# Kernel tuning notes

Measured on AMD Instinct MI355X. Metric: run time of the kernel, lower is better.

Reference implementation:

```python
import jax, jax.numpy as jnp
import numpy as np

EPS = 1e-6
TOP_K = 2


def setup_inputs() -> dict:
    key = jax.random.key(0)
    k0, k1, k2, k3, k4 = jax.random.split(key, 5)
    B, S, H, I, E = 1, 2048, 1024, 3584, 8
    return {
        "hidden_states": jax.random.normal(k0, (B, S, H), jnp.float32),
        "rms_weight": jnp.ones((H,), jnp.float32),
        "gate_w": jax.random.normal(k1, (E, H), jnp.float32) * (H ** -0.5),
        "w1": jax.random.normal(k2, (E, I, H), jnp.float32) * (H ** -0.5),
        "w2": jax.random.normal(k3, (E, H, I), jnp.float32) * (I ** -0.5),
        "w3": jax.random.normal(k4, (E, I, H), jnp.float32) * (H ** -0.5),
    }


def reference(hidden_states, rms_weight, gate_w, w1, w2, w3):
    B, S, H = hidden_states.shape
    E = gate_w.shape[0]
    # RMSNorm (fp32 internally, matches _RMSNorm)
    x = hidden_states.astype(jnp.float32)
    var = jnp.mean(x * x, axis=-1, keepdims=True)
    h = rms_weight * (x * jax.lax.rsqrt(var + EPS))  # [B,S,H]
    # Router: softmax over experts, top-k, renormalize
    logits = jnp.einsum('bsh,eh->bse', h, gate_w)
    scores = jax.nn.softmax(logits.astype(jnp.float32), axis=-1)
    top_w, top_i = jax.lax.top_k(scores, TOP_K)        # [B,S,K]
    top_w = top_w / jnp.sum(top_w, axis=-1, keepdims=True)
    top_w = top_w.astype(h.dtype)
    # Per-token combine weight for every expert: cw[t,e]
    hf = h.reshape(-1, H)                               # [T,H]
    oh = jax.nn.one_hot(top_i.reshape(-1, TOP_K), E, dtype=h.dtype)  # [T,K,E]
    cw = jnp.einsum('tke,tk->te', oh, top_w.reshape(-1, TOP_K))       # [T,E]
    # SwiGLU expert MLPs, batched over experts (dense dispatch; weights zero out unrouted tokens)
    a = jnp.einsum('th,eih->eti', hf, w1)               # [E,T,I]
    g = jnp.einsum('th,eih->eti', hf, w3)               # [E,T,I]
    eo = jnp.einsum('eti,ehi->eth', jax.nn.silu(a) * g, w2)  # [E,T,H]
    out = jnp.einsum('eth,te->th', eo, cw)              # [T,H]
    return hidden_states + out.reshape(B, S, H)
```

## Files before the change

kernel.cpp:

```cpp
#include <hip/hip_runtime.h>
#include <hip/hip_bf16.h>
#include <stdint.h>

#define T_TOK 2048
#define HDIM  1024
#define IDIM  3584
#define NEXP  8
#define NROWS 4096
#define WELEM 29360128
#define NJOBS 40
#define CVTB  512

typedef __attribute__((ext_vector_type(8))) short bf16x8;
typedef __attribute__((ext_vector_type(4))) float f32x4;

typedef __attribute__((address_space(3))) unsigned lds_u32;
typedef const __attribute__((address_space(1))) unsigned glb_u32;

#define MFMA16 __builtin_amdgcn_mfma_f32_16x16x32_bf16

__device__ __forceinline__ unsigned short f2bf(float f){
  union { float f; unsigned u; } v; v.f = f;
  unsigned r = v.u + 0x7FFFu + ((v.u >> 16) & 1u);
  return (unsigned short)(r >> 16);
}
__device__ __forceinline__ unsigned cvt2(float a, float b){
  __hip_bfloat162 h = __float22bfloat162_rn(float2{a, b});
  return *reinterpret_cast<unsigned*>(&h);
}
__device__ __forceinline__ bf16x8 pack8(float4 lo, float4 hi){
  union { __hip_bfloat162 b2[4]; bf16x8 v; } u;
  u.b2[0] = __float22bfloat162_rn(float2{lo.x, lo.y});
  u.b2[1] = __float22bfloat162_rn(float2{lo.z, lo.w});
  u.b2[2] = __float22bfloat162_rn(float2{hi.x, hi.y});
  u.b2[3] = __float22bfloat162_rn(float2{hi.z, hi.w});
  return u.v;
}

__global__ __launch_bounds__(256) void k_rms_router(
    const float* __restrict__ x, const float* __restrict__ rmsw,
    const float* __restrict__ gw, unsigned short* __restrict__ h_bf,
    int* __restrict__ topk_i, float* __restrict__ topk_w, int* __restrict__ count)
{
  const int t = blockIdx.x, tid = threadIdx.x;
  const int lane = tid & 63, wid = tid >> 6;
  float4 x4 = reinterpret_cast<const float4*>(x)[t*256 + tid];
  float ss = x4.x*x4.x + x4.y*x4.y + x4.z*x4.z + x4.w*x4.w;
  #pragma unroll
  for (int o = 32; o >= 1; o >>= 1) ss += __shfl_xor(ss, o);
  __shared__ float sred[4];
  __shared__ float slog[32];
  if (lane == 0) sred[wid] = ss;
  __syncthreads();
  float inv = rsqrtf((sred[0]+sred[1]+sred[2]+sred[3]) * (1.0f/HDIM) + 1e-6f);
  float4 w4 = reinterpret_cast<const float4*>(rmsw)[tid];
  float h0 = x4.x*inv*w4.x, h1 = x4.y*inv*w4.y, h2 = x4.z*inv*w4.z, h3 = x4.w*inv*w4.w;
  ushort4 hb; hb.x = f2bf(h0); hb.y = f2bf(h1); hb.z = f2bf(h2); hb.w = f2bf(h3);
  reinterpret_cast<ushort4*>(h_bf)[t*256 + tid] = hb;
  #pragma unroll
  for (int e = 0; e < NEXP; e++){
    float4 g4 = reinterpret_cast<const float4*>(gw)[e*256 + tid];
    float v = h0*g4.x + h1*g4.y + h2*g4.z + h3*g4.w;
    #pragma unroll
    for (int o = 32; o >= 1; o >>= 1) v += __shfl_xor(v, o);
    if (lane == 0) slog[e*4 + wid] = v;
  }
  __syncthreads();
  if (tid == 0){
    float lg[NEXP];
    #pragma unroll
    for (int e = 0; e < NEXP; e++) lg[e] = slog[e*4]+slog[e*4+1]+slog[e*4+2]+slog[e*4+3];
    int i0 = 0;
    for (int e = 1; e < NEXP; e++) if (lg[e] > lg[i0]) i0 = e;
    int i1 = -1;
    for (int e = 0; e < NEXP; e++){ if (e == i0) continue; if (i1 < 0 || lg[e] > lg[i1]) i1 = e; }
    float m  = fmaxf(lg[i0], lg[i1]);
    float e0 = expf(lg[i0]-m), e1 = expf(lg[i1]-m);
    float s  = e0 + e1;
    topk_i[t*2] = i0; topk_i[t*2+1] = i1;
    topk_w[t*2] = e0/s; topk_w[t*2+1] = e1/s;
    atomicAdd(&count[i0], 1); atomicAdd(&count[i1], 1);
  }
}

__global__ void k_scan(const int* __restrict__ count, int* __restrict__ offset,
                       int* __restrict__ jobs){
  if (threadIdx.x == 0){
    int o = 0, L = 0;
    for (int e = 0; e < NEXP; e++){
      offset[e] = o;
      int nrt = (count[e] + 127) >> 7;
      for (int r = 0; r < nrt && L < NJOBS; r++) jobs[L++] = (e << 8) | r;
      o += count[e];
    }
    for (; L < NJOBS; L++) jobs[L] = -1;
  }
}

__global__ __launch_bounds__(256) void k_scatter(
    const int* __restrict__ topk_i, const float* __restrict__ topk_w,
    const int* __restrict__ offset, int* __restrict__ cursor,
    int* __restrict__ token_of_row, float* __restrict__ wrow, int* __restrict__ slot_of)
{
  int t = blockIdx.x*256 + threadIdx.x;
  if (t >= T_TOK) return;
  #pragma unroll
  for (int k = 0; k < 2; k++){
    int e = topk_i[t*2+k];
    int pos = atomicAdd(&cursor[e], 1);
    int row = offset[e] + pos;
    token_of_row[row] = t;
    wrow[row] = topk_w[t*2+k];
    slot_of[t*2+k] = row;
  }
}

__global__ __launch_bounds__(256) void k_cvt(
    const float4* __restrict__ src, uint2* __restrict__ dst, int n4)
{
  int stride = gridDim.x * blockDim.x;
  for (int i = blockIdx.x*blockDim.x + threadIdx.x; i < n4; i += stride){
    float4 v = src[i];
    dst[i] = make_uint2(cvt2(v.x, v.y), cvt2(v.z, v.w));
  }
}

__global__ __launch_bounds__(256, 3) void k_mlp_in(
    const unsigned short* __restrict__ h_bf, const float* __restrict__ w1,
    const float* __restrict__ w3, const int* __restrict__ token_of_row,
    const int* __restrict__ count, const int* __restrict__ offset,
    const int* __restrict__ jobs, unsigned short* __restrict__ act,
    const float4* __restrict__ w2s, uint2* __restrict__ w2d)
{
  const int d = blockIdx.x;
  const int tid = threadIdx.x;
  if (d >= NJOBS*56){
    if (w2d){
      int i0 = (d - NJOBS*56)*256 + tid;
      for (int i = i0; i < WELEM/4; i += CVTB*256){
        float4 v = w2s[i];
        w2d[i] = make_uint2(cvt2(v.x, v.y), cvt2(v.z, v.w));
      }
    }
    return;
  }
  const int p = d % 56;
  const int t = d / 56;
  const int job = jobs[t];
  if (job < 0) return;
  const int e = job >> 8, rt = job & 255;
  const int cnt = count[e];
  const int off = offset[e], row0 = off + rt*128, rend = off + cnt;
  const int col0 = p * 64;
  const int lane = tid & 63, wid = tid >> 6;
  const int wave_r = wid >> 1, wave_c = wid & 1;

  __shared__ __align__(16) char sA [16384];
  __shared__ __align__(16) char sB1[16384];
  __shared__ __align__(16) char sB3[16384];

  const int srow = tid >> 3;
  const int sg   = (tid & 7) ^ (srow & 7);
  const unsigned short* aptr[4];
  #pragma unroll
  for (int j = 0; j < 4; j++){
    int tok = token_of_row[min(row0 + srow + 32*j, NROWS-1)];
    aptr[j] = h_bf + (size_t)tok*HDIM + sg*8;
  }
  const int bl = (tid & 15) ^ ((tid >> 4) & 15);
  const float* b1base = w1 + ((size_t)e*IDIM + col0 + (tid >> 4))*HDIM + bl*4;
  const float* b3base = w3 + ((size_t)e*IDIM + col0 + (tid >> 4))*HDIM + bl*4;

  #define ISSUE(kk) {                                                                \
    _Pragma("unroll")                                                                \
    for (int j = 0; j < 4; j++)                                                      \
      __builtin_amdgcn_global_load_lds((glb_u32*)(const void*)(aptr[j] + (kk)*64),   \
          (lds_u32*)(void*)(sA + j*4096 + tid*16), 16, 0, 0);                        \
    _Pragma("unroll")                                                                \
    for (int j = 0; j < 4; j++){                                                     \
      __builtin_amdgcn_global_load_lds(                                              \
          (glb_u32*)(const void*)(b1base + (size_t)j*16*HDIM + (kk)*64),             \
          (lds_u32*)(void*)(sB1 + j*4096 + tid*16), 16, 0, 0);                       \
      __builtin_amdgcn_global_load_lds(                                              \
          (glb_u32*)(const void*)(b3base + (size_t)j*16*HDIM + (kk)*64),             \
          (lds_u32*)(void*)(sB3 + j*4096 + tid*16), 16, 0, 0);                       \
    } }

  f32x4 acc1[4][2], acc3[4][2];
  #pragma unroll
  for (int m = 0; m < 4; m++)
    #pragma unroll
    for (int n = 0; n < 2; n++){
      acc1[m][n] = (f32x4){0.f,0.f,0.f,0.f};
      acc3[m][n] = (f32x4){0.f,0.f,0.f,0.f};
    }

  for (int kk = 0; kk < HDIM/64; kk++){
    ISSUE(kk);
    __syncthreads();
    #pragma unroll
    for (int ki = 0; ki < 2; ki++){
      bf16x8 af[4];
      #pragma unroll
      for (int m = 0; m < 4; m++){
        int row = wave_r*64 + m*16 + (lane & 15);
        int slot = ki*4 + (lane >> 4);
        af[m] = *reinterpret_cast<const bf16x8*>(sA + row*128 + ((slot ^ (row&7))<<4));
      }
      #pragma unroll
      for (int n = 0; n < 2; n++){
        int c  = wave_c*32 + n*16 + (lane & 15);
        int l0 = ki*8 + (lane >> 4)*2;
        int p0 = (l0     ^ (c & 15)) << 4;
        int p1 = ((l0+1) ^ (c & 15)) << 4;
        float4 lo1 = *reinterpret_cast<const float4*>(sB1 + c*256 + p0);
        float4 hi1 = *reinterpret_cast<const float4*>(sB1 + c*256 + p1);
        float4 lo3 = *reinterpret_cast<const float4*>(sB3 + c*256 + p0);
        float4 hi3 = *reinterpret_cast<const float4*>(sB3 + c*256 + p1);
        bf16x8 b1 = pack8(lo1, hi1);
        bf16x8 b3 = pack8(lo3, hi3);
        #pragma unroll
        for (int m = 0; m < 4; m++){
          acc1[m][n] = MFMA16(af[m], b1, acc1[m][n], 0,0,0);
          acc3[m][n] = MFMA16(af[m], b3, acc3[m][n], 0,0,0);
        }
      }
    }
    __syncthreads();
  }

  const int lcol = lane & 15, lrow4 = (lane >> 4) * 4;
  #pragma unroll
  for (int m = 0; m < 4; m++){
    #pragma unroll
    for (int n = 0; n < 2; n++){
      int gcol = col0 + wave_c*32 + n*16 + lcol;
      #pragma unroll
      for (int r = 0; r < 4; r++){
        int grow = row0 + wave_r*64 + m*16 + lrow4 + r;
        if (grow < rend){
          float a = acc1[m][n][r], g = acc3[m][n][r];
          float sig = 1.0f / (1.0f + __expf(-a));
          act[(size_t)grow*IDIM + gcol] = f2bf(a * sig * g);
        }
      }
    }
  }
  #undef ISSUE
}

__global__ __launch_bounds__(256, 3) void k_mlp_out(
    const unsigned short* __restrict__ act, const unsigned short* __restrict__ w2bf,
    const float* __restrict__ wrow, const int* __restrict__ count,
    const int* __restrict__ offset, const int* __restrict__ jobs,
    float* __restrict__ eo)
{
  const int d = blockIdx.x;
  const int p = d & 15;
  const int t = d >> 4;
  const int job = jobs[t];
  if (job < 0) return;
  const int e = job >> 8, rt = job & 255;
  const int cnt = count[e];
  const int off = offset[e], row0 = off + rt*128, rend = off + cnt;
  const int col0 = p * 64;
  const int tid = threadIdx.x, lane = tid & 63, wid = tid >> 6;
  const int wave_r = wid >> 1, wave_c = wid & 1;

  __shared__ __align__(16) char sA[32768];
  __shared__ __align__(16) char sB[16384];

  const int sr16 = tid >> 4;
  const int sg   = (tid & 15) ^ sr16;

  const unsigned short* aptr[8];
  #pragma unroll
  for (int j = 0; j < 8; j++){
    int r = min(row0 + j*16 + sr16, NROWS-1);
    aptr[j] = act + (size_t)r*IDIM + sg*8;
  }
  const unsigned short* bptr[4];
  #pragma unroll
  for (int j = 0; j < 4; j++){
    int col = col0 + j*16 + sr16;
    bptr[j] = w2bf + (size_t)(e*HDIM + col)*IDIM + sg*8;
  }

  #define ISSUE(kk) {                                                                \
    _Pragma("unroll")                                                                \
    for (int j = 0; j < 8; j++)                                                      \
      __builtin_amdgcn_global_load_lds((glb_u32*)(const void*)(aptr[j] + (kk)*128),  \
          (lds_u32*)(void*)(sA + j*4096 + tid*16), 16, 0, 0);                        \
    _Pragma("unroll")                                                                \
    for (int j = 0; j < 4; j++)                                                      \
      __builtin_amdgcn_global_load_lds((glb_u32*)(const void*)(bptr[j] + (kk)*128),  \
          (lds_u32*)(void*)(sB + j*4096 + tid*16), 16, 0, 0); }

  f32x4 acc[4][2];
  #pragma unroll
  for (int m = 0; m < 4; m++)
    #pragma unroll
    for (int n = 0; n < 2; n++) acc[m][n] = (f32x4){0.f,0.f,0.f,0.f};

  for (int kk = 0; kk < IDIM/128; kk++){
    ISSUE(kk);
    __syncthreads();
    #pragma unroll
    for (int ki = 0; ki < 4; ki++){
      bf16x8 af[4];
      #pragma unroll
      for (int m = 0; m < 4; m++){
        int row = wave_r*64 + m*16 + (lane & 15);
        int slot = ki*4 + (lane >> 4);
        af[m] = *reinterpret_cast<const bf16x8*>(sA + row*256 + ((slot ^ (row&15))<<4));
      }
      #pragma unroll
      for (int n = 0; n < 2; n++){
        int col = wave_c*32 + n*16 + (lane & 15);
        int slot = ki*4 + (lane >> 4);
        bf16x8 fb = *reinterpret_cast<const bf16x8*>(sB + col*256 + ((slot ^ (col&15))<<4));
        #pragma unroll
        for (int m = 0; m < 4; m++)
          acc[m][n] = MFMA16(af[m], fb, acc[m][n], 0,0,0);
      }
    }
    __syncthreads();
  }

  const int lcol = lane & 15, lrow4 = (lane >> 4) * 4;
  #pragma unroll
  for (int m = 0; m < 4; m++){
    #pragma unroll
    for (int n = 0; n < 2; n++){
      int gcol = col0 + wave_c*32 + n*16 + lcol;
      #pragma unroll
      for (int r = 0; r < 4; r++){
        int grow = row0 + wave_r*64 + m*16 + lrow4 + r;
        if (grow < rend){
          eo[(size_t)grow*HDIM + gcol] = acc[m][n][r] * wrow[grow];
        }
      }
    }
  }
  #undef ISSUE
}

__global__ __launch_bounds__(256) void k_combine(
    const float* __restrict__ x, const float* __restrict__ eo,
    const int* __restrict__ slot_of, float* __restrict__ out)
{
  const int t = blockIdx.x, tid = threadIdx.x;
  const int s0 = slot_of[t*2], s1 = slot_of[t*2+1];
  float4 xv = reinterpret_cast<const float4*>(x)[t*256 + tid];
  float4 a  = reinterpret_cast<const float4*>(eo)[s0*256 + tid];
  float4 b  = reinterpret_cast<const float4*>(eo)[s1*256 + tid];
  float4 ov;
  ov.x = xv.x + a.x + b.x;
  ov.y = xv.y + a.y + b.y;
  ov.z = xv.z + a.z + b.z;
  ov.w = xv.w + a.w + b.w;
  reinterpret_cast<float4*>(out)[t*256 + tid] = ov;
}

extern "C" void kernel_launch(void* const* d_in, const int* in_sizes, int n_in,
                              void* d_out, int out_size, void* d_ws, size_t ws_size,
                              hipStream_t stream)
{
  const float* x    = (const float*)d_in[0];
  const float* rmsw = (const float*)d_in[1];
  const float* gw   = (const float*)d_in[2];
  const float* w1   = (const float*)d_in[3];
  const float* w2   = (const float*)d_in[4];
  const float* w3   = (const float*)d_in[5];
  float* out = (float*)d_out;

  char* ws = (char*)d_ws;
  size_t o = 0;
  auto alloc = [&](size_t bytes) -> void* {
    void* p = ws + o;
    o += (bytes + 255) & ~(size_t)255;
    return p;
  };
  unsigned short* h_bf   = (unsigned short*)alloc((size_t)T_TOK*HDIM*2);
  int*   topk_i          = (int*)  alloc(T_TOK*2*4);
  float* topk_w          = (float*)alloc(T_TOK*2*4);
  int*   counters        = (int*)  alloc(64*4);
  int*   jobs            = (int*)  alloc(NJOBS*4);
  int*   token_of_row    = (int*)  alloc(NROWS*4);
  float* wrow            = (float*)alloc(NROWS*4);
  int*   slot_of         = (int*)  alloc(T_TOK*2*4);
  unsigned short* act    = (unsigned short*)alloc((size_t)NROWS*IDIM*2);
  float* eo              = (float*)alloc((size_t)NROWS*HDIM*4);
  int* count  = counters;
  int* cursor = counters + 8;
  int* offset = counters + 16;

  bool havew2 = (ws_size >= o + (size_t)WELEM*2);
  unsigned short* w2bf = (unsigned short*)(ws + o);

  hipMemsetAsync(counters, 0, 64*4, stream);
  k_rms_router<<<T_TOK, 256, 0, stream>>>(x, rmsw, gw, h_bf, topk_i, topk_w, count);
  k_scan<<<1, 64, 0, stream>>>(count, offset, jobs);
  k_scatter<<<(T_TOK+255)/256, 256, 0, stream>>>(topk_i, topk_w, offset, cursor,
                                                 token_of_row, wrow, slot_of);
  k_mlp_in<<<NJOBS*56 + (havew2 ? CVTB : 0), 256, 0, stream>>>(
      h_bf, w1, w3, token_of_row, count, offset, jobs, act,
      (const float4*)w2, havew2 ? (uint2*)w2bf : (uint2*)nullptr);
  if (!havew2)
    k_cvt<<<2048, 256, 0, stream>>>((const float4*)w2, (uint2*)w2bf, WELEM/4);
  k_mlp_out<<<NJOBS*16, 256, 0, stream>>>(act, w2bf, wrow, count, offset, jobs, eo);
  k_combine<<<T_TOK, 256, 0, stream>>>(x, eo, slot_of, out);
}
```

Before: 297.7 us.

## Double-buffer A tiles and prefetch fp32 weights through registers into bf16 LDS

The gate/up expert GEMM kernel now double-buffers the activation tile in LDS using asynchronous global-to-LDS loads. The fp32 w1/w3 tiles are prefetched into registers one K-step ahead and converted to bf16 once when written to LDS. Before, each wave re-read fp32 from LDS and converted it in the inner loop. This halves LDS footprint and traffic for B and overlaps global loads with MFMA work. The custom barrier only waits on lgkmcnt, so it relies on the compiler's vmcnt handling to make sure the async A loads are complete before they are read, which is a correctness risk.

```diff
diff --git a/kernel.cpp b/kernel.cpp
--- a/kernel.cpp
+++ b/kernel.cpp
@@ -35,6 +35,13 @@
   u.b2[2] = __float22bfloat162_rn(float2{hi.x, hi.y});
   u.b2[3] = __float22bfloat162_rn(float2{hi.z, hi.w});
   return u.v;
+}
+
+__device__ __forceinline__ void pub_barrier(){
+  asm volatile("s_waitcnt lgkmcnt(0)" ::: "memory");
+  __builtin_amdgcn_sched_barrier(0);
+  __builtin_amdgcn_s_barrier();
+  __builtin_amdgcn_sched_barrier(0);
 }
 
 __global__ __launch_bounds__(256) void k_rms_router(
@@ -155,9 +162,9 @@
   const int lane = tid & 63, wid = tid >> 6;
   const int wave_r = wid >> 1, wave_c = wid & 1;
 
-  __shared__ __align__(16) char sA [16384];
-  __shared__ __align__(16) char sB1[16384];
-  __shared__ __align__(16) char sB3[16384];
+  __shared__ __align__(16) char sA [2*16384];
+  __shared__ __align__(16) char sB1[8192];
+  __shared__ __align__(16) char sB2[8192];
 
   const int srow = tid >> 3;
   const int sg   = (tid & 7) ^ (srow & 7);
@@ -167,23 +174,27 @@
     int tok = token_of_row[min(row0 + srow + 32*j, NROWS-1)];
     aptr[j] = h_bf + (size_t)tok*HDIM + sg*8;
   }
-  const int bl = (tid & 15) ^ ((tid >> 4) & 15);
-  const float* b1base = w1 + ((size_t)e*IDIM + col0 + (tid >> 4))*HDIM + bl*4;
-  const float* b3base = w3 + ((size_t)e*IDIM + col0 + (tid >> 4))*HDIM + bl*4;
-
-  #define ISSUE(kk) {                                                                \
-    _Pragma("unroll")                                                                \
+  #define ISSUE_A(kk, b) { _Pragma("unroll")                                         \
     for (int j = 0; j < 4; j++)                                                      \
       __builtin_amdgcn_global_load_lds((glb_u32*)(const void*)(aptr[j] + (kk)*64),   \
-          (lds_u32*)(void*)(sA + j*4096 + tid*16), 16, 0, 0);                        \
-    _Pragma("unroll")                                                                \
-    for (int j = 0; j < 4; j++){                                                     \
-      __builtin_amdgcn_global_load_lds(                                              \
-          (glb_u32*)(const void*)(b1base + (size_t)j*16*HDIM + (kk)*64),             \
-          (lds_u32*)(void*)(sB1 + j*4096 + tid*16), 16, 0, 0);                       \
-      __builtin_amdgcn_global_load_lds(                                              \
-          (glb_u32*)(const void*)(b3base + (size_t)j*16*HDIM + (kk)*64),             \
-          (lds_u32*)(void*)(sB3 + j*4096 + tid*16), 16, 0, 0);                       \
+          (lds_u32*)(void*)(sA + (b)*16384 + j*4096 + tid*16), 16, 0, 0); }
+
+  const int kseg = tid & 7;
+  const float* w1base = w1 + (size_t)(e*IDIM + col0 + srow)*HDIM + kseg*8;
+  const float* w3base = w3 + (size_t)(e*IDIM + col0 + srow)*HDIM + kseg*8;
+  float4 pb1[2][2], pb3[2][2];
+  #define LOAD_B(kk) { _Pragma("unroll")                                             \
+    for (int j = 0; j < 2; j++){                                                     \
+      const float4* p1 = reinterpret_cast<const float4*>(w1base + (size_t)(32*j)*HDIM + (kk)*64); \
+      const float4* p3 = reinterpret_cast<const float4*>(w3base + (size_t)(32*j)*HDIM + (kk)*64); \
+      pb1[j][0] = p1[0]; pb1[j][1] = p1[1];                                          \
+      pb3[j][0] = p3[0]; pb3[j][1] = p3[1];                                          \
+    } }
+  const int bswz = (kseg ^ (srow & 7)) << 4;
+  #define STORE_B() { _Pragma("unroll")                                              \
+    for (int j = 0; j < 2; j++){                                                     \
+      *reinterpret_cast<bf16x8*>(sB1 + (srow + 32*j)*128 + bswz) = pack8(pb1[j][0], pb1[j][1]); \
+      *reinterpret_cast<bf16x8*>(sB2 + (srow + 32*j)*128 + bswz) = pack8(pb3[j][0], pb3[j][1]); \
     } }
 
   f32x4 acc1[4][2], acc3[4][2];
@@ -195,38 +206,40 @@
       acc3[m][n] = (f32x4){0.f,0.f,0.f,0.f};
     }
 
-  for (int kk = 0; kk < HDIM/64; kk++){
-    ISSUE(kk);
-    __syncthreads();
-    #pragma unroll
-    for (int ki = 0; ki < 2; ki++){
-      bf16x8 af[4];
-      #pragma unroll
-      for (int m = 0; m < 4; m++){
-        int row = wave_r*64 + m*16 + (lane & 15);
-        int slot = ki*4 + (lane >> 4);
-        af[m] = *reinterpret_cast<const bf16x8*>(sA + row*128 + ((slot ^ (row&7))<<4));
-      }
-      #pragma unroll
-      for (int n = 0; n < 2; n++){
-        int c  = wave_c*32 + n*16 + (lane & 15);
-        int l0 = ki*8 + (lane >> 4)*2;
-        int p0 = (l0     ^ (c & 15)) << 4;
-        int p1 = ((l0+1) ^ (c & 15)) << 4;
-        float4 lo1 = *reinterpret_cast<const float4*>(sB1 + c*256 + p0);
-        float4 hi1 = *reinterpret_cast<const float4*>(sB1 + c*256 + p1);
-        float4 lo3 = *reinterpret_cast<const float4*>(sB3 + c*256 + p0);
-        float4 hi3 = *reinterpret_cast<const float4*>(sB3 + c*256 + p1);
-        bf16x8 b1 = pack8(lo1, hi1);
-        bf16x8 b3 = pack8(lo3, hi3);
-        #pragma unroll
-        for (int m = 0; m < 4; m++){
-          acc1[m][n] = MFMA16(af[m], b1, acc1[m][n], 0,0,0);
-          acc3[m][n] = MFMA16(af[m], b3, acc3[m][n], 0,0,0);
-        }
-      }
-    }
-    __syncthreads();
+  #define COMPUTE(b) { _Pragma("unroll")                                             \
+    for (int ki = 0; ki < 2; ki++){                                                  \
+      bf16x8 af[4];                                                                  \
+      _Pragma("unroll")                                                              \
+      for (int m = 0; m < 4; m++){                                                   \
+        int row = wave_r*64 + m*16 + (lane & 15);                                    \
+        int slot = ki*4 + (lane >> 4);                                               \
+        af[m] = *reinterpret_cast<const bf16x8*>(sA + (b)*16384 + row*128 + ((slot ^ (row&7))<<4)); \
+      }                                                                              \
+      _Pragma("unroll")                                                              \
+      for (int n = 0; n < 2; n++){                                                   \
+        int col = wave_c*32 + n*16 + (lane & 15);                                    \
+        int slot = ki*4 + (lane >> 4);                                               \
+        bf16x8 b1 = *reinterpret_cast<const bf16x8*>(sB1 + col*128 + ((slot ^ (col&7))<<4)); \
+        bf16x8 b2 = *reinterpret_cast<const bf16x8*>(sB2 + col*128 + ((slot ^ (col&7))<<4)); \
+        _Pragma("unroll")                                                            \
+        for (int m = 0; m < 4; m++){                                                 \
+          acc1[m][n] = MFMA16(af[m], b1, acc1[m][n], 0,0,0);                         \
+          acc3[m][n] = MFMA16(af[m], b2, acc3[m][n], 0,0,0);                         \
+        }                                                                            \
+      }                                                                              \
+    } }
+
+  const int NK = HDIM/64;
+  ISSUE_A(0, 0);
+  LOAD_B(0);
+  for (int kk = 0; kk < NK; kk++){
+    const int b = kk & 1;
+    if (kk + 1 < NK) ISSUE_A(kk+1, b^1);
+    STORE_B();
+    if (kk + 1 < NK) LOAD_B(kk+1);
+    pub_barrier();
+    COMPUTE(b);
+    pub_barrier();
   }
 
   const int lcol = lane & 15, lrow4 = (lane >> 4) * 4;
@@ -246,7 +259,10 @@
       }
     }
   }
-  #undef ISSUE
+  #undef ISSUE_A
+  #undef LOAD_B
+  #undef STORE_B
+  #undef COMPUTE
 }
 
 __global__ __launch_bounds__(256, 3) void k_mlp_out(
```

Result: slower. 308.4 us (+3.6%).
